# Kernel tuning notes

Measured on AMD Instinct MI355X. Metric: run time of the kernel, lower is better.

## Reference

```python
import jax, jax.numpy as jnp
import numpy as np

N = 10000          # nodes
DEG = 16           # incoming edges per node
E = N * DEG
D_IN = 2048        # backbone embed dim
RED = 4
D = D_IN // RED    # 512, gnn embed dim
NHEAD = 8
HD = D // NHEAD    # 64
DHID = 4 * D       # 2048, mlp hidden
L = 2              # num gnn layers
NCLS = 751
EPS = 1e-5


def _layernorm(x, g, b):
    m = jnp.mean(x, axis=-1, keepdims=True)
    v = jnp.var(x, axis=-1, keepdims=True)
    return (x - m) * jax.lax.rsqrt(v + EPS) * g + b


def _attention_layer(feats, r, c, Wq, bq, Wk, bk, Wv, bv, Wo, bo,
                     g1, be1, W1, b1, W2, b2, g2, be2):
    # MultiHeadDotProduct (dropout = identity in eval, mult_attr=0)
    q = (feats @ Wq.T + bq).reshape(N, NHEAD, HD)
    k = (feats @ Wk.T + bk).reshape(N, NHEAD, HD)
    v = (feats @ Wv.T + bv).reshape(N, NHEAD, HD)
    # per-edge scores: q gathered at target c, k gathered at source r
    scores = jnp.einsum('ehd,ehd->eh', q[c], k[r]) / np.float32(np.sqrt(HD))  # [E,H]
    # segment softmax grouped by target node c
    mx = jax.ops.segment_max(scores, c, num_segments=N)          # [N,H]
    ex = jnp.exp(scores - mx[c])
    den = jax.ops.segment_sum(ex, c, num_segments=N)             # [N,H]
    alpha = ex / den[c]                                          # [E,H]
    # weighted scatter-add of source values (aggr='add')
    agg = jax.ops.segment_sum(alpha[:, :, None] * v[r], c, num_segments=N)  # [N,H,HD]
    f2 = agg.reshape(N, D) @ Wo.T + bo
    # DotAttentionLayer: res1 + norm1 + mlp + res2 + norm2
    feats = _layernorm(feats + f2, g1, be1)
    f2 = jax.nn.relu(feats @ W1.T + b1) @ W2.T + b2
    return _layernorm(feats + f2, g2, be2)


def setup_inputs() -> dict:
    key = jax.random.key(0)
    ks = jax.random.split(key, 24)
    feats = jax.random.normal(ks[0], (N, D_IN), jnp.float32)
    # edge list: each target node c has DEG incoming edges from random sources r
    c = jnp.repeat(jnp.arange(N, dtype=jnp.int64), DEG)
    r = jax.random.randint(ks[1], (E,), 0, N, dtype=jnp.int64)
    edge_index = jnp.stack([r, c], axis=1)                       # [E,2]
    edge_attr = jax.random.uniform(ks[2], (E, 1), jnp.float32)
    s = 0.02
    inp = {
        'feats': feats, 'edge_index': edge_index, 'edge_attr': edge_attr,
        'Wred': jax.random.normal(ks[3], (D, D_IN), jnp.float32) * s,
        'bred': jnp.zeros((D,), jnp.float32),
        'Wq': jax.random.normal(ks[4], (L, D, D), jnp.float32) * s,
        'bq': jnp.zeros((L, D), jnp.float32),
        'Wk': jax.random.normal(ks[5], (L, D, D), jnp.float32) * s,
        'bk': jnp.zeros((L, D), jnp.float32),
        'Wv': jax.random.normal(ks[6], (L, D, D), jnp.float32) * s,
        'bv': jnp.zeros((L, D), jnp.float32),
        'Wo': jax.random.normal(ks[7], (L, D, D), jnp.float32) * s,
        'bo': jnp.zeros((L, D), jnp.float32),
        'g1': jnp.ones((L, D), jnp.float32),
        'be1': jnp.zeros((L, D), jnp.float32),
        'W1': jax.random.normal(ks[8], (L, DHID, D), jnp.float32) * s,
        'b1': jnp.zeros((L, DHID), jnp.float32),
        'W2': jax.random.normal(ks[9], (L, D, DHID), jnp.float32) * s,
        'b2': jnp.zeros((L, D), jnp.float32),
        'g2': jnp.ones((L, D), jnp.float32),
        'be2': jnp.zeros((L, D), jnp.float32),
        'bn_g': jnp.ones((D,), jnp.float32),
        'bn_b': jnp.zeros((D,), jnp.float32),
        'Wfc': jax.random.normal(ks[10], (NCLS, D), jnp.float32) * s,
    }
    return inp


def reference(feats, edge_index, edge_attr, Wred, bred, Wq, bq, Wk, bk, Wv, bv,
              Wo, bo, g1, be1, W1, b1, W2, b2, g2, be2, bn_g, bn_b, Wfc):
    r, c = edge_index[:, 0], edge_index[:, 1]
    # dim_red
    x = feats @ Wred.T + bred                                    # [N,D]
    # GNNNetwork: stacked DotAttentionLayers (out list, last taken since cat=0, every=0)
    for i in range(L):
        x = _attention_layer(x, r, c, Wq[i], bq[i], Wk[i], bk[i], Wv[i], bv[i],
                             Wo[i], bo[i], g1[i], be1[i], W1[i], b1[i],
                             W2[i], b2[i], g2[i], be2[i])
    feats_out = x
    # neck=1: BatchNorm1d in eval (running_mean=0, running_var=1) then bias-free fc
    bn = (feats_out * jax.lax.rsqrt(jnp.float32(1.0 + EPS))) * bn_g + bn_b
    logits = bn @ Wfc.T                                          # [N,NCLS]
    return (logits, feats_out)
```

## Files before the change

### kernel.cpp

```cpp
#include <hip/hip_runtime.h>
#include <hip/hip_bf16.h>

#define MPAD   10112
#define NR     10000
#define DM     512
#define DH     2048
#define DIN    2048
#define NCLS   751

typedef __attribute__((ext_vector_type(8))) short bf16x8;
typedef __attribute__((ext_vector_type(4))) float f32x4;
typedef __attribute__((address_space(3))) void lds_t;
typedef const __attribute__((address_space(1))) void glb_t;

static __device__ __forceinline__ float bf2f(unsigned short s) {
    union { unsigned u; float f; } c; c.u = ((unsigned)s) << 16; return c.f;
}
static __device__ __forceinline__ unsigned short f2bf(float f) {
    __hip_bfloat16 h = __float2bfloat16(f);
    return __builtin_bit_cast(unsigned short, h);
}

__global__ __launch_bounds__(256) void cvt8(
    const float* s0, const float* s1, const float* s2, const float* s3,
    const float* s4, const float* s5, const float* s6, const float* s7,
    unsigned short* d0, unsigned short* d1, unsigned short* d2, unsigned short* d3,
    unsigned short* d4, unsigned short* d5, unsigned short* d6, unsigned short* d7,
    int n0, int n1, int n2, int n3, int n4, int n5, int n6, int n7)
{
    const float* s; unsigned short* d; int n;
    switch (blockIdx.y) {
        case 0: s = s0; d = d0; n = n0; break;
        case 1: s = s1; d = d1; n = n1; break;
        case 2: s = s2; d = d2; n = n2; break;
        case 3: s = s3; d = d3; n = n3; break;
        case 4: s = s4; d = d4; n = n4; break;
        case 5: s = s5; d = d5; n = n5; break;
        case 6: s = s6; d = d6; n = n6; break;
        default: s = s7; d = d7; n = n7; break;
    }
    const int idx = (blockIdx.x * 256 + threadIdx.x) * 8;
    if (idx >= n) return;
    float4 a = *(const float4*)(s + idx);
    float4 b = *(const float4*)(s + idx + 4);
    union { unsigned short us[8]; int4 v; } o;
    o.us[0] = f2bf(a.x); o.us[1] = f2bf(a.y); o.us[2] = f2bf(a.z); o.us[3] = f2bf(a.w);
    o.us[4] = f2bf(b.x); o.us[5] = f2bf(b.y); o.us[6] = f2bf(b.z); o.us[7] = f2bf(b.w);
    *(int4*)(d + idx) = o.v;
}

__global__ __launch_bounds__(256) void catbias(
    const float* __restrict__ bq, const float* __restrict__ bk,
    const float* __restrict__ bv, float* __restrict__ bqkv)
{
    const int t = blockIdx.x * 256 + threadIdx.x;
    if (t >= 2 * 3 * DM) return;
    const int l = t / (3 * DM), j = t % (3 * DM);
    float v;
    if (j < DM)          v = bq[l * DM + j];
    else if (j < 2 * DM) v = bk[l * DM + j - DM];
    else                 v = bv[l * DM + j - 2 * DM];
    bqkv[t] = v;
}

__global__ __launch_bounds__(256) void pad_feats(
    const float* __restrict__ f, unsigned short* __restrict__ h)
{
    const size_t t = (size_t)blockIdx.x * 256 + threadIdx.x;
    const size_t idx = t * 8;
    const int row = (int)(idx / DIN);
    union { unsigned short us[8]; int4 v; } o;
    if (row < NR) {
        float4 a = *(const float4*)(f + idx);
        float4 b = *(const float4*)(f + idx + 4);
        o.us[0] = f2bf(a.x); o.us[1] = f2bf(a.y); o.us[2] = f2bf(a.z); o.us[3] = f2bf(a.w);
        o.us[4] = f2bf(b.x); o.us[5] = f2bf(b.y); o.us[6] = f2bf(b.z); o.us[7] = f2bf(b.w);
    } else {
        o.v = (int4){0, 0, 0, 0};
    }
    *(int4*)(h + idx) = o.v;
}

static __device__ __forceinline__ int xcd_swizzle(int nwg) {
    const int d0  = blockIdx.y * gridDim.x + blockIdx.x;
    const int xcd = d0 & 7, dd = d0 >> 3;
    const int qc  = nwg >> 3, rc = nwg & 7;
    return (xcd < rc ? xcd * (qc + 1) : rc * (qc + 1) + (xcd - rc) * qc) + dd;
}


template<int EPI, bool GUARD>
__global__ __launch_bounds__(256) void gemm_bt(
    const unsigned short* __restrict__ A,
    const unsigned short* __restrict__ B,
    const float* __restrict__ bias,
    float* __restrict__ outF,
    unsigned short* __restrict__ outH,
    int K, int Nw, int ldc, int Mreal, int Nreal)
{
    __shared__ short As[128 * 64];
    __shared__ short Bs[128 * 64];
    const int tid  = threadIdx.x;
    const int lane = tid & 63;
    const int w    = tid >> 6;
    const int wm   = w >> 1, wn = w & 1;

    const int wgid = xcd_swizzle(gridDim.x * gridDim.y);
    const int bm0 = (wgid / gridDim.x) * 128;
    const int bn0 = (wgid % gridDim.x) * 128;

    f32x4 acc[4][4];
    #pragma unroll
    for (int i = 0; i < 4; ++i)
        #pragma unroll
        for (int j = 0; j < 4; ++j) acc[i][j] = (f32x4){0.f, 0.f, 0.f, 0.f};

    const int srow = lane >> 3;
    const int sslot = ((lane & 7) ^ srow) * 8;
    const int fr   = lane & 15;
    const int fr7  = fr & 7;
    const int c16  = lane >> 4;
    const int nkt  = K >> 6;

    for (int kt = 0; kt < nkt; ++kt) {
        if (kt) __syncthreads();
        #pragma unroll
        for (int c = 0; c < 4; ++c) {
            const int rb = c * 32 + w * 8;
            const int r  = rb + srow;
            const unsigned short* sa = A + (size_t)(bm0 + r) * K + kt * 64 + sslot;
            __builtin_amdgcn_global_load_lds((glb_t*)sa, (lds_t*)&As[rb * 64], 16, 0, 0);
            int br = bn0 + r; if (br >= Nw) br = Nw - 1;
            const unsigned short* sb = B + (size_t)br * K + kt * 64 + sslot;
            __builtin_amdgcn_global_load_lds((glb_t*)sb, (lds_t*)&Bs[rb * 64], 16, 0, 0);
        }
        __syncthreads();
        #pragma unroll
        for (int kk = 0; kk < 64; kk += 32) {
            const int slot = (((kk >> 3) + c16) ^ fr7) * 8;
            bf16x8 av[4], bv[4];
            #pragma unroll
            for (int mi = 0; mi < 4; ++mi)
                av[mi] = *(const bf16x8*)&As[(wm * 64 + mi * 16 + fr) * 64 + slot];
            #pragma unroll
            for (int ni = 0; ni < 4; ++ni)
                bv[ni] = *(const bf16x8*)&Bs[(wn * 64 + ni * 16 + fr) * 64 + slot];
            #pragma unroll
            for (int mi = 0; mi < 4; ++mi)
                #pragma unroll
                for (int ni = 0; ni < 4; ++ni)
                    acc[mi][ni] = __builtin_amdgcn_mfma_f32_16x16x32_bf16(
                        av[mi], bv[ni], acc[mi][ni], 0, 0, 0);
        }
    }

    const int rg = (lane >> 4) * 4;
    #pragma unroll
    for (int mi = 0; mi < 4; ++mi) {
        #pragma unroll
        for (int ni = 0; ni < 4; ++ni) {
            const int col = bn0 + wn * 64 + ni * 16 + fr;
            const int bcol = col < Nw ? col : Nw - 1;
            const float bvv = (EPI == 4) ? 0.f : bias[bcol];
            const f32x4 v = acc[mi][ni];
            #pragma unroll
            for (int j = 0; j < 4; ++j) {
                const int row = bm0 + wm * 64 + mi * 16 + rg + j;
                float val = v[j] + bvv;
                if (EPI == 3) val = fmaxf(val, 0.f);
                if (GUARD && (row >= Mreal || col >= Nreal)) continue;
                const size_t idx = (size_t)row * ldc + col;
                if (EPI == 0 || EPI == 1 || EPI == 4) outF[idx] = val;
                if (EPI == 1 || EPI == 2 || EPI == 3) outH[idx] = f2bf(val);
            }
        }
    }
}

template<int EPI, bool GUARD>
__global__ __launch_bounds__(256) void gemm_bt64(
    const unsigned short* __restrict__ A,
    const unsigned short* __restrict__ B,
    const float* __restrict__ bias,
    float* __restrict__ outF,
    unsigned short* __restrict__ outH,
    int K, int Nw, int ldc, int Mreal, int Nreal)
{
    __shared__ short As[64 * 64];
    __shared__ short Bs[64 * 64];
    const int tid  = threadIdx.x;
    const int lane = tid & 63;
    const int w    = tid >> 6;
    const int wm   = w >> 1, wn = w & 1;

    const int wgid = xcd_swizzle(gridDim.x * gridDim.y);
    const int bm0 = (wgid / gridDim.x) * 64;
    const int bn0 = (wgid % gridDim.x) * 64;

    f32x4 acc[2][2];
    #pragma unroll
    for (int i = 0; i < 2; ++i)
        #pragma unroll
        for (int j = 0; j < 2; ++j) acc[i][j] = (f32x4){0.f, 0.f, 0.f, 0.f};

    const int srow = lane >> 3;
    const int sslot = ((lane & 7) ^ srow) * 8;
    const int fr   = lane & 15;
    const int fr7  = fr & 7;
    const int c16  = lane >> 4;
    const int nkt  = K >> 6;

    for (int kt = 0; kt < nkt; ++kt) {
        if (kt) __syncthreads();
        #pragma unroll
        for (int c = 0; c < 2; ++c) {
            const int rb = c * 32 + w * 8;
            const int r  = rb + srow;
            const unsigned short* sa = A + (size_t)(bm0 + r) * K + kt * 64 + sslot;
            __builtin_amdgcn_global_load_lds((glb_t*)sa, (lds_t*)&As[rb * 64], 16, 0, 0);
            int br = bn0 + r; if (br >= Nw) br = Nw - 1;
            const unsigned short* sb = B + (size_t)br * K + kt * 64 + sslot;
            __builtin_amdgcn_global_load_lds((glb_t*)sb, (lds_t*)&Bs[rb * 64], 16, 0, 0);
        }
        __syncthreads();
        #pragma unroll
        for (int kk = 0; kk < 64; kk += 32) {
            const int slot = (((kk >> 3) + c16) ^ fr7) * 8;
            bf16x8 av[2], bv[2];
            #pragma unroll
            for (int mi = 0; mi < 2; ++mi)
                av[mi] = *(const bf16x8*)&As[(wm * 32 + mi * 16 + fr) * 64 + slot];
            #pragma unroll
            for (int ni = 0; ni < 2; ++ni)
                bv[ni] = *(const bf16x8*)&Bs[(wn * 32 + ni * 16 + fr) * 64 + slot];
            #pragma unroll
            for (int mi = 0; mi < 2; ++mi)
                #pragma unroll
                for (int ni = 0; ni < 2; ++ni)
                    acc[mi][ni] = __builtin_amdgcn_mfma_f32_16x16x32_bf16(
                        av[mi], bv[ni], acc[mi][ni], 0, 0, 0);
        }
    }

    const int rg = (lane >> 4) * 4;
    #pragma unroll
    for (int mi = 0; mi < 2; ++mi) {
        #pragma unroll
        for (int ni = 0; ni < 2; ++ni) {
            const int col = bn0 + wn * 32 + ni * 16 + fr;
            const int bcol = col < Nw ? col : Nw - 1;
            const float bvv = (EPI == 4) ? 0.f : bias[bcol];
            const f32x4 v = acc[mi][ni];
            #pragma unroll
            for (int j = 0; j < 4; ++j) {
                const int row = bm0 + wm * 32 + mi * 16 + rg + j;
                float val = v[j] + bvv;
                if (EPI == 3) val = fmaxf(val, 0.f);
                if (GUARD && (row >= Mreal || col >= Nreal)) continue;
                const size_t idx = (size_t)row * ldc + col;
                if (EPI == 0 || EPI == 1 || EPI == 4) outF[idx] = val;
                if (EPI == 1 || EPI == 2 || EPI == 3) outH[idx] = f2bf(val);
            }
        }
    }
}

__global__ __launch_bounds__(256) void attn_kernel(
    const unsigned short* __restrict__ qkv,
    const int* __restrict__ ei,
    unsigned short* __restrict__ aggb)
{
    const int wid  = threadIdx.x >> 6;
    const int lane = threadIdx.x & 63;
    const int iout = blockIdx.x * 4 + wid;
    const int i    = iout < NR ? iout : NR - 1;
    const int stride = (ei[33] == 0) ? 4 : 2;

    __shared__ int   sr[4][16];
    __shared__ float ssc[4][16 * 8];
    __shared__ float sal[4][16 * 8];

    bf16x8 qv = *(const bf16x8*)(qkv + (size_t)i * 1536 + lane * 8);
    float qf[8];
    #pragma unroll
    for (int j = 0; j < 8; ++j) qf[j] = bf2f((unsigned short)qv[j]);

    if (lane < 16) sr[wid][lane] = ei[((size_t)i * 16 + lane) * stride];
    __syncthreads();

    const int hh = lane >> 3;
    #pragma unroll 4
    for (int e = 0; e < 16; ++e) {
        const int r = sr[wid][e];
        bf16x8 kv = *(const bf16x8*)(qkv + (size_t)r * 1536 + DM + lane * 8);
        float dot = 0.f;
        #pragma unroll
        for (int j = 0; j < 8; ++j) dot += qf[j] * bf2f((unsigned short)kv[j]);
        dot += __shfl_xor(dot, 1, 64);
        dot += __shfl_xor(dot, 2, 64);
        dot += __shfl_xor(dot, 4, 64);
        if ((lane & 7) == 0) ssc[wid][e * 8 + hh] = dot * 0.125f;
    }
    __syncthreads();
    if (lane < 8) {
        float mx = -1e30f;
        for (int e = 0; e < 16; ++e) mx = fmaxf(mx, ssc[wid][e * 8 + lane]);
        float den = 0.f, ex[16];
        for (int e = 0; e < 16; ++e) { ex[e] = expf(ssc[wid][e * 8 + lane] - mx); den += ex[e]; }
        const float inv = 1.f / den;
        for (int e = 0; e < 16; ++e) sal[wid][e * 8 + lane] = ex[e] * inv;
    }
    __syncthreads();
    float accv[8] = {0, 0, 0, 0, 0, 0, 0, 0};
    #pragma unroll 4
    for (int e = 0; e < 16; ++e) {
        const int r = sr[wid][e];
        const float al = sal[wid][e * 8 + hh];
        bf16x8 vv = *(const bf16x8*)(qkv + (size_t)r * 1536 + 2 * DM + lane * 8);
        #pragma unroll
        for (int j = 0; j < 8; ++j) accv[j] += al * bf2f((unsigned short)vv[j]);
    }
    union { unsigned short us[8]; int4 v4; } o;
    if (iout < NR) {
        #pragma unroll
        for (int j = 0; j < 8; ++j) o.us[j] = f2bf(accv[j]);
    } else {
        o.v4 = (int4){0, 0, 0, 0};
    }
    *(int4*)(aggb + (size_t)iout * DM + lane * 8) = o.v4;
}

__global__ __launch_bounds__(64) void ln_kernel(
    float* __restrict__ x, const float* __restrict__ f2,
    const float* __restrict__ g, const float* __restrict__ be,
    unsigned short* __restrict__ xb)
{
    const int row = blockIdx.x;
    const int lane = threadIdx.x;
    float* xp = x + (size_t)row * DM + lane * 8;
    const float* fp = f2 + (size_t)row * DM + lane * 8;
    float v[8];
    float4 a0 = *(const float4*)xp;
    float4 a1 = *(const float4*)(xp + 4);
    float4 b0 = *(const float4*)fp;
    float4 b1 = *(const float4*)(fp + 4);
    v[0]=a0.x+b0.x; v[1]=a0.y+b0.y; v[2]=a0.z+b0.z; v[3]=a0.w+b0.w;
    v[4]=a1.x+b1.x; v[5]=a1.y+b1.y; v[6]=a1.z+b1.z; v[7]=a1.w+b1.w;
    float s = 0.f, s2 = 0.f;
    #pragma unroll
    for (int j = 0; j < 8; ++j) { s += v[j]; s2 += v[j] * v[j]; }
    #pragma unroll
    for (int off = 32; off > 0; off >>= 1) {
        s  += __shfl_xor(s, off, 64);
        s2 += __shfl_xor(s2, off, 64);
    }
    const float mean = s * (1.f / DM);
    const float var  = s2 * (1.f / DM) - mean * mean;
    const float rs   = rsqrtf(var + 1e-5f);
    float y[8];
    union { unsigned short us[8]; int4 v4; } o;
    #pragma unroll
    for (int j = 0; j < 8; ++j) {
        const int d = lane * 8 + j;
        y[j] = (v[j] - mean) * rs * g[d] + be[d];
        o.us[j] = f2bf(y[j]);
    }
    float4 w0 = {y[0], y[1], y[2], y[3]}, w1 = {y[4], y[5], y[6], y[7]};
    *(float4*)xp = w0; *(float4*)(xp + 4) = w1;
    *(int4*)(xb + (size_t)row * DM + lane * 8) = o.v4;
}

__global__ __launch_bounds__(64) void final_bn(
    const float* __restrict__ x,
    const float* __restrict__ g, const float* __restrict__ b,
    unsigned short* __restrict__ xb, float* __restrict__ outFeats)
{
    const int row = blockIdx.x;
    const int lane = threadIdx.x;
    const float s = rsqrtf(1.f + 1e-5f);
    const float* xp = x + (size_t)row * DM + lane * 8;
    union { unsigned short us[8]; int4 v4; } o;
    float f[8];
    #pragma unroll
    for (int j = 0; j < 8; ++j) {
        const int d = lane * 8 + j;
        const float xv = xp[j];
        o.us[j] = f2bf(xv * s * g[d] + b[d]);
        f[j] = xv;
    }
    *(int4*)(xb + (size_t)row * DM + lane * 8) = o.v4;
    if (row < NR) {
        float4 f0 = {f[0], f[1], f[2], f[3]}, f1 = {f[4], f[5], f[6], f[7]};
        float* op = outFeats + (size_t)row * DM + lane * 8;
        *(float4*)op = f0; *(float4*)(op + 4) = f1;
    }
}

extern "C" void kernel_launch(void* const* d_in, const int* in_sizes, int n_in,
                              void* d_out, int out_size, void* d_ws, size_t ws_size,
                              hipStream_t stream)
{
    const float* feats = (const float*)d_in[0];
    const int* ei = (const int*)d_in[1];
    const float* Wred = (const float*)d_in[3];
    const float* bred = (const float*)d_in[4];
    const float* Wq = (const float*)d_in[5];
    const float* bq = (const float*)d_in[6];
    const float* Wk = (const float*)d_in[7];
    const float* bk = (const float*)d_in[8];
    const float* Wv = (const float*)d_in[9];
    const float* bv = (const float*)d_in[10];
    const float* Wo = (const float*)d_in[11];
    const float* bo = (const float*)d_in[12];
    const float* g1 = (const float*)d_in[13];
    const float* be1 = (const float*)d_in[14];
    const float* W1 = (const float*)d_in[15];
    const float* b1 = (const float*)d_in[16];
    const float* W2 = (const float*)d_in[17];
    const float* b2 = (const float*)d_in[18];
    const float* g2 = (const float*)d_in[19];
    const float* be2 = (const float*)d_in[20];
    const float* bng = (const float*)d_in[21];
    const float* bnb = (const float*)d_in[22];
    const float* Wfc = (const float*)d_in[23];

    char* ws = (char*)d_ws;
    size_t off = 0;
    auto alloc = [&](size_t bytes) {
        void* p = ws + off; off += (bytes + 255) & ~(size_t)255; return p;
    };
    unsigned short* h    = (unsigned short*)alloc((size_t)MPAD * DIN * 2);
    unsigned short* xb   = (unsigned short*)alloc((size_t)MPAD * DM * 2);
    unsigned short* qkvb = (unsigned short*)alloc((size_t)MPAD * 3 * DM * 2);
    unsigned short* aggb = (unsigned short*)alloc((size_t)MPAD * DM * 2);
    float* x   = (float*)alloc((size_t)MPAD * DM * 4);
    float* tmp = (float*)alloc((size_t)MPAD * DM * 4);
    unsigned short* wredB = (unsigned short*)alloc((size_t)DM * DIN * 2);
    unsigned short* wqkvB = (unsigned short*)alloc((size_t)2 * 3 * DM * DM * 2);
    unsigned short* woB   = (unsigned short*)alloc((size_t)2 * DM * DM * 2);
    unsigned short* w1B   = (unsigned short*)alloc((size_t)2 * DH * DM * 2);
    unsigned short* w2B   = (unsigned short*)alloc((size_t)2 * DM * DH * 2);
    unsigned short* wfcB  = (unsigned short*)alloc((size_t)NCLS * DM * 2);
    float* bqkv = (float*)alloc((size_t)2 * 3 * DM * 4);

    const int MT  = MPAD / 128;
    const int MT2 = MPAD / 64;
    const int QK  = DM * DM;

    cvt8<<<dim3(QK / 8 / 256, 8), 256, 0, stream>>>(
        Wq, Wk, Wv, Wq + QK, Wk + QK, Wv + QK, nullptr, nullptr,
        wqkvB, wqkvB + QK, wqkvB + 2 * QK, wqkvB + 3 * QK, wqkvB + 4 * QK, wqkvB + 5 * QK,
        nullptr, nullptr,
        QK, QK, QK, QK, QK, QK, 0, 0);
    cvt8<<<dim3(2 * DH * DM / 8 / 256, 8), 256, 0, stream>>>(
        Wred, Wo, W1, W2, Wfc, nullptr, nullptr, nullptr,
        wredB, woB, w1B, w2B, wfcB, nullptr, nullptr, nullptr,
        DM * DIN, 2 * DM * DM, 2 * DH * DM, 2 * DM * DH, NCLS * DM, 0, 0, 0);
    catbias<<<(2 * 3 * DM + 255) / 256, 256, 0, stream>>>(bq, bk, bv, bqkv);
    pad_feats<<<MPAD * DIN / 8 / 256, 256, 0, stream>>>(feats, h);

    gemm_bt64<1, false><<<dim3(DM / 64, MT2), 256, 0, stream>>>(
        h, wredB, bred, x, xb, DIN, DM, DM, MPAD, DM);

    for (int l = 0; l < 2; ++l) {
        const size_t bOff = (size_t)l * DM;
        gemm_bt<2, false><<<dim3(12, MT), 256, 0, stream>>>(
            xb, wqkvB + (size_t)l * 3 * QK, bqkv + (size_t)l * 3 * DM,
            nullptr, qkvb, DM, 3 * DM, 3 * DM, MPAD, 3 * DM);
        attn_kernel<<<MPAD / 4, 256, 0, stream>>>(qkvb, ei, aggb);
        gemm_bt64<0, false><<<dim3(DM / 64, MT2), 256, 0, stream>>>(
            aggb, woB + (size_t)l * QK, bo + bOff, tmp, nullptr, DM, DM, DM, MPAD, DM);
        ln_kernel<<<MPAD, 64, 0, stream>>>(x, tmp, g1 + bOff, be1 + bOff, xb);
        gemm_bt<3, false><<<dim3(16, MT), 256, 0, stream>>>(
            xb, w1B + (size_t)l * DH * DM, b1 + (size_t)l * DH, nullptr, h, DM, DH, DH, MPAD, DH);
        gemm_bt64<0, false><<<dim3(DM / 64, MT2), 256, 0, stream>>>(
            h, w2B + (size_t)l * DM * DH, b2 + bOff, tmp, nullptr, DH, DM, DM, MPAD, DM);
        ln_kernel<<<MPAD, 64, 0, stream>>>(x, tmp, g2 + bOff, be2 + bOff, xb);
    }

    float* out = (float*)d_out;
    final_bn<<<MPAD, 64, 0, stream>>>(x, bng, bnb, xb, out + (size_t)NR * NCLS);
    gemm_bt64<4, true><<<dim3((NCLS + 63) / 64, MT2), 256, 0, stream>>>(
        xb, wfcB, nullptr, out, nullptr, DM, NCLS, NCLS, NR, NCLS);

    (void)in_sizes; (void)n_in; (void)out_size; (void)ws_size;
}
```

Before: 437.3 us.

## Fold eval BatchNorm into FC weights and emit bf16 GEMM outputs before LayerNorm

```diff
diff --git a/kernel.cpp b/kernel.cpp
--- a/kernel.cpp
+++ b/kernel.cpp
@@ -47,6 +47,36 @@
     o.us[0] = f2bf(a.x); o.us[1] = f2bf(a.y); o.us[2] = f2bf(a.z); o.us[3] = f2bf(a.w);
     o.us[4] = f2bf(b.x); o.us[5] = f2bf(b.y); o.us[6] = f2bf(b.z); o.us[7] = f2bf(b.w);
     *(int4*)(d + idx) = o.v;
+}
+
+__global__ __launch_bounds__(256) void cvt_fc(
+    const float* __restrict__ Wfc, const float* __restrict__ g,
+    unsigned short* __restrict__ out)
+{
+    const int idx = (blockIdx.x * 256 + threadIdx.x) * 8;
+    if (idx >= NCLS * DM) return;
+    const float s = rsqrtf(1.f + 1e-5f);
+    union { unsigned short us[8]; int4 v; } o;
+    #pragma unroll
+    for (int j = 0; j < 8; ++j)
+        o.us[j] = f2bf(Wfc[idx + j] * s * g[(idx + j) & (DM - 1)]);
+    *(int4*)(out + idx) = o.v;
+}
+
+__global__ __launch_bounds__(64) void bnfc_bias(
+    const float* __restrict__ Wfc, const float* __restrict__ bnb,
+    float* __restrict__ biasfc)
+{
+    const int c = blockIdx.x;
+    const int lane = threadIdx.x;
+    const float* wp = Wfc + (size_t)c * DM + lane * 8;
+    const float* bp = bnb + lane * 8;
+    float s = 0.f;
+    #pragma unroll
+    for (int j = 0; j < 8; ++j) s += wp[j] * bp[j];
+    #pragma unroll
+    for (int off = 32; off > 0; off >>= 1) s += __shfl_xor(s, off, 64);
+    if (lane == 0) biasfc[c] = s;
 }
 
 __global__ __launch_bounds__(256) void catbias(
@@ -331,21 +361,22 @@
 }
 
 __global__ __launch_bounds__(64) void ln_kernel(
-    float* __restrict__ x, const float* __restrict__ f2,
+    float* __restrict__ x, const unsigned short* __restrict__ f2,
     const float* __restrict__ g, const float* __restrict__ be,
-    unsigned short* __restrict__ xb)
+    unsigned short* __restrict__ xb, float* __restrict__ outFeats)
 {
     const int row = blockIdx.x;
     const int lane = threadIdx.x;
     float* xp = x + (size_t)row * DM + lane * 8;
-    const float* fp = f2 + (size_t)row * DM + lane * 8;
+    const unsigned short* fp = f2 + (size_t)row * DM + lane * 8;
     float v[8];
     float4 a0 = *(const float4*)xp;
     float4 a1 = *(const float4*)(xp + 4);
-    float4 b0 = *(const float4*)fp;
-    float4 b1 = *(const float4*)(fp + 4);
-    v[0]=a0.x+b0.x; v[1]=a0.y+b0.y; v[2]=a0.z+b0.z; v[3]=a0.w+b0.w;
-    v[4]=a1.x+b1.x; v[5]=a1.y+b1.y; v[6]=a1.z+b1.z; v[7]=a1.w+b1.w;
+    bf16x8 fv = *(const bf16x8*)fp;
+    v[0]=a0.x; v[1]=a0.y; v[2]=a0.z; v[3]=a0.w;
+    v[4]=a1.x; v[5]=a1.y; v[6]=a1.z; v[7]=a1.w;
+    #pragma unroll
+    for (int j = 0; j < 8; ++j) v[j] += bf2f((unsigned short)fv[j]);
     float s = 0.f, s2 = 0.f;
     #pragma unroll
     for (int j = 0; j < 8; ++j) { s += v[j]; s2 += v[j] * v[j]; }
@@ -368,31 +399,9 @@
     float4 w0 = {y[0], y[1], y[2], y[3]}, w1 = {y[4], y[5], y[6], y[7]};
     *(float4*)xp = w0; *(float4*)(xp + 4) = w1;
     *(int4*)(xb + (size_t)row * DM + lane * 8) = o.v4;
-}
-
-__global__ __launch_bounds__(64) void final_bn(
-    const float* __restrict__ x,
-    const float* __restrict__ g, const float* __restrict__ b,
-    unsigned short* __restrict__ xb, float* __restrict__ outFeats)
-{
-    const int row = blockIdx.x;
-    const int lane = threadIdx.x;
-    const float s = rsqrtf(1.f + 1e-5f);
-    const float* xp = x + (size_t)row * DM + lane * 8;
-    union { unsigned short us[8]; int4 v4; } o;
-    float f[8];
-    #pragma unroll
-    for (int j = 0; j < 8; ++j) {
-        const int d = lane * 8 + j;
-        const float xv = xp[j];
-        o.us[j] = f2bf(xv * s * g[d] + b[d]);
-        f[j] = xv;
-    }
-    *(int4*)(xb + (size_t)row * DM + lane * 8) = o.v4;
-    if (row < NR) {
-        float4 f0 = {f[0], f[1], f[2], f[3]}, f1 = {f[4], f[5], f[6], f[7]};
+    if (outFeats != nullptr && row < NR) {
         float* op = outFeats + (size_t)row * DM + lane * 8;
-        *(float4*)op = f0; *(float4*)(op + 4) = f1;
+        *(float4*)op = w0; *(float4*)(op + 4) = w1;
     }
 }
 
@@ -433,19 +442,22 @@
     unsigned short* xb   = (unsigned short*)alloc((size_t)MPAD * DM * 2);
     unsigned short* qkvb = (unsigned short*)alloc((size_t)MPAD * 3 * DM * 2);
     unsigned short* aggb = (unsigned short*)alloc((size_t)MPAD * DM * 2);
+    unsigned short* tmpH = (unsigned short*)alloc((size_t)MPAD * DM * 2);
     float* x   = (float*)alloc((size_t)MPAD * DM * 4);
-    float* tmp = (float*)alloc((size_t)MPAD * DM * 4);
     unsigned short* wredB = (unsigned short*)alloc((size_t)DM * DIN * 2);
     unsigned short* wqkvB = (unsigned short*)alloc((size_t)2 * 3 * DM * DM * 2);
     unsigned short* woB   = (unsigned short*)alloc((size_t)2 * DM * DM * 2);
     unsigned short* w1B   = (unsigned short*)alloc((size_t)2 * DH * DM * 2);
     unsigned short* w2B   = (unsigned short*)alloc((size_t)2 * DM * DH * 2);
     unsigned short* wfcB  = (unsigned short*)alloc((size_t)NCLS * DM * 2);
-    float* bqkv = (float*)alloc((size_t)2 * 3 * DM * 4);
+    float* bqkv   = (float*)alloc((size_t)2 * 3 * DM * 4);
+    float* biasfc = (float*)alloc((size_t)NCLS * 4);
 
     const int MT  = MPAD / 128;
     const int MT2 = MPAD / 64;
     const int QK  = DM * DM;
+
+    float* out = (float*)d_out;
 
     cvt8<<<dim3(QK / 8 / 256, 8), 256, 0, stream>>>(
         Wq, Wk, Wv, Wq + QK, Wk + QK, Wv + QK, nullptr, nullptr,
@@ -453,9 +465,11 @@
         nullptr, nullptr,
         QK, QK, QK, QK, QK, QK, 0, 0);
     cvt8<<<dim3(2 * DH * DM / 8 / 256, 8), 256, 0, stream>>>(
-        Wred, Wo, W1, W2, Wfc, nullptr, nullptr, nullptr,
-        wredB, woB, w1B, w2B, wfcB, nullptr, nullptr, nullptr,
-        DM * DIN, 2 * DM * DM, 2 * DH * DM, 2 * DM * DH, NCLS * DM, 0, 0, 0);
+        Wred, Wo, W1, W2, nullptr, nullptr, nullptr, nullptr,
+        wredB, woB, w1B, w2B, nullptr, nullptr, nullptr, nullptr,
+        DM * DIN, 2 * DM * DM, 2 * DH * DM, 2 * DM * DH, 0, 0, 0, 0);
+    cvt_fc<<<(NCLS * DM / 8 + 255) / 256, 256, 0, stream>>>(Wfc, bng, wfcB);
+    bnfc_bias<<<NCLS, 64, 0, stream>>>(Wfc, bnb, biasfc);
     catbias<<<(2 * 3 * DM + 255) / 256, 256, 0, stream>>>(bq, bk, bv, bqkv);
     pad_feats<<<MPAD * DIN / 8 / 256, 256, 0, stream>>>(feats, h);
 
@@ -468,20 +482,19 @@
             xb, wqkvB + (size_t)l * 3 * QK, bqkv + (size_t)l * 3 * DM,
             nullptr, qkvb, DM, 3 * DM, 3 * DM, MPAD, 3 * DM);
         attn_kernel<<<MPAD / 4, 256, 0, stream>>>(qkvb, ei, aggb);
-        gemm_bt64<0, false><<<dim3(DM / 64, MT2), 256, 0, stream>>>(
-            aggb, woB + (size_t)l * QK, bo + bOff, tmp, nullptr, DM, DM, DM, MPAD, DM);
-        ln_kernel<<<MPAD, 64, 0, stream>>>(x, tmp, g1 + bOff, be1 + bOff, xb);
+        gemm_bt64<2, false><<<dim3(DM / 64, MT2), 256, 0, stream>>>(
+            aggb, woB + (size_t)l * QK, bo + bOff, nullptr, tmpH, DM, DM, DM, MPAD, DM);
+        ln_kernel<<<MPAD, 64, 0, stream>>>(x, tmpH, g1 + bOff, be1 + bOff, xb, nullptr);
         gemm_bt<3, false><<<dim3(16, MT), 256, 0, stream>>>(
             xb, w1B + (size_t)l * DH * DM, b1 + (size_t)l * DH, nullptr, h, DM, DH, DH, MPAD, DH);
-        gemm_bt64<0, false><<<dim3(DM / 64, MT2), 256, 0, stream>>>(
-            h, w2B + (size_t)l * DM * DH, b2 + bOff, tmp, nullptr, DH, DM, DM, MPAD, DM);
-        ln_kernel<<<MPAD, 64, 0, stream>>>(x, tmp, g2 + bOff, be2 + bOff, xb);
-    }
-
-    float* out = (float*)d_out;
-    final_bn<<<MPAD, 64, 0, stream>>>(x, bng, bnb, xb, out + (size_t)NR * NCLS);
-    gemm_bt64<4, true><<<dim3((NCLS + 63) / 64, MT2), 256, 0, stream>>>(
-        xb, wfcB, nullptr, out, nullptr, DM, NCLS, NCLS, NR, NCLS);
+        gemm_bt64<2, false><<<dim3(DM / 64, MT2), 256, 0, stream>>>(
+            h, w2B + (size_t)l * DM * DH, b2 + bOff, nullptr, tmpH, DH, DM, DM, MPAD, DM);
+        ln_kernel<<<MPAD, 64, 0, stream>>>(x, tmpH, g2 + bOff, be2 + bOff, xb,
+                                           (l == 1) ? out + (size_t)NR * NCLS : nullptr);
+    }
+
+    gemm_bt64<0, true><<<dim3((NCLS + 63) / 64, MT2), 256, 0, stream>>>(
+        xb, wfcB, biasfc, out, nullptr, DM, NCLS, NCLS, NR, NCLS);
 
     (void)in_sizes; (void)n_in; (void)out_size; (void)ws_size;
 }
```

Measured after the change: 438.5 us. Within noise of the previous version (+0.3%).
